# Performance work log

Measured on AMD Instinct MI355X. Metric: run time of the kernel, lower is better.

## Reference

```python
import jax, jax.numpy as jnp
import numpy as np
import math

D_MODEL = 2048
B, S, PAST = 4, 2048, 2048


def setup_inputs() -> dict:
    key = jax.random.key(0)
    ks = jax.random.split(key, 8)
    scale = 0.02
    x = jax.random.normal(ks[0], (B, S, D_MODEL), dtype=jnp.float32)
    past_k = jax.random.normal(ks[1], (B, PAST, D_MODEL), dtype=jnp.float32)
    past_v = jax.random.normal(ks[2], (B, PAST, D_MODEL), dtype=jnp.float32)
    Wq = jax.random.normal(ks[3], (D_MODEL, D_MODEL), dtype=jnp.float32) * scale
    Wk = jax.random.normal(ks[4], (D_MODEL, D_MODEL), dtype=jnp.float32) * scale
    Wv = jax.random.normal(ks[5], (D_MODEL, D_MODEL), dtype=jnp.float32) * scale
    Wo = jax.random.normal(ks[6], (D_MODEL, D_MODEL), dtype=jnp.float32) * scale
    bq = jnp.zeros((D_MODEL,), jnp.float32)
    bk = jnp.zeros((D_MODEL,), jnp.float32)
    bv = jnp.zeros((D_MODEL,), jnp.float32)
    bo = jnp.zeros((D_MODEL,), jnp.float32)
    return {"x": x, "past_k": past_k, "past_v": past_v,
            "Wq": Wq, "bq": bq, "Wk": Wk, "bk": bk,
            "Wv": Wv, "bv": bv, "Wo": Wo, "bo": bo}


def reference(x, past_k, past_v, Wq, bq, Wk, bk, Wv, bv, Wo, bo):
    d_model = x.shape[-1]
    # torch Linear: y = x @ W.T + b; here W is stored [out, in] equivalently square
    q = jnp.einsum('bsd,ed->bse', x, Wq) + bq
    k = jnp.einsum('bsd,ed->bse', x, Wk) + bk
    v = jnp.einsum('bsd,ed->bse', x, Wv) + bv
    k_cache = jnp.concatenate([past_k, k], axis=1)  # [B, PAST+S, D]
    v_cache = jnp.concatenate([past_v, v], axis=1)
    scores = jnp.einsum('bqd,bkd->bqk', q, k_cache) / math.sqrt(d_model)
    weights = jax.nn.softmax(scores, axis=-1)
    attn = jnp.einsum('bqk,bkd->bqd', weights, v_cache)
    out = jnp.einsum('bqd,ed->bqe', attn, Wo) + bo
    return out, (k_cache, v_cache)
```

## Files before the change

### kernel.cpp

```cpp
#include <hip/hip_runtime.h>
#include <math.h>

typedef unsigned short u16;
typedef __bf16 bf16x8 __attribute__((ext_vector_type(8)));
typedef float f32x4 __attribute__((ext_vector_type(4)));
typedef short s16x8 __attribute__((ext_vector_type(8)));

#define DM 2048
#define NB 4
#define SEQ 2048
#define PAST_N 2048
#define CS 4096

__device__ __forceinline__ u16 f2bf(float f) {
  unsigned u = __float_as_uint(f);
  u += 0x7fff + ((u >> 16) & 1);
  return (u16)(u >> 16);
}
__device__ __forceinline__ float bf2f(u16 h) {
  return __uint_as_float(((unsigned)h) << 16);
}

__device__ __forceinline__ void gl_lds16(const u16* g, u16* l) {
  __builtin_amdgcn_global_load_lds(
      (const __attribute__((address_space(1))) unsigned*)g,
      (__attribute__((address_space(3))) unsigned*)l, 16, 0, 0);
}

__device__ __forceinline__ bf16x8 ldsfrag(const u16* s, int row, int colb) {
  const int byte_off = (row * 128 + colb) ^ ((row & 7) << 4);
  return *(const bf16x8*)((const char*)s + byte_off);
}

__device__ __forceinline__ void stage4(const u16* __restrict__ g, int ld,
                                       u16* lwb, int t) {
#pragma unroll
  for (int j = 0; j < 4; ++j) {
    const int c = j * 512 + t;
    const int row = c >> 3;
    const int slot = (c & 7) ^ (row & 7);
    gl_lds16(g + (long)row * ld + slot * 8, lwb + j * 4096);
  }
}

#define LOADA(mh)                                                       \
  _Pragma("unroll") for (int mi = 0; mi < 4; ++mi) {                    \
    const int rwa = wr * 128 + ((mh) * 4 + mi) * 16 + lr;               \
    a[mi][0] = ldsfrag(sA, rwa, kb0);                                   \
    a[mi][1] = ldsfrag(sA, rwa, 64 + kb0);                              \
  }

#define LOADB(nh)                                                       \
  _Pragma("unroll") for (int ni = 0; ni < 2; ++ni) {                    \
    const int rwb = wc * 64 + ((nh) * 2 + ni) * 16 + lr;                \
    b[ni][0] = ldsfrag(sB, rwb, kb0);                                   \
    b[ni][1] = ldsfrag(sB, rwb, 64 + kb0);                              \
  }

#define MM(mh, nh)                                                      \
  _Pragma("unroll") for (int kk = 0; kk < 2; ++kk)                      \
  _Pragma("unroll") for (int mi = 0; mi < 4; ++mi)                      \
  _Pragma("unroll") for (int ni = 0; ni < 2; ++ni)                      \
    acc[(mh) * 4 + mi][(nh) * 2 + ni] =                                 \
        __builtin_amdgcn_mfma_f32_16x16x32_bf16(                        \
            a[mi][kk], b[ni][kk], acc[(mh) * 4 + mi][(nh) * 2 + ni],    \
            0, 0, 0);

#define PHASE_SYNC                                                      \
  __builtin_amdgcn_s_barrier();                                         \
  asm volatile("s_waitcnt lgkmcnt(0)" ::: "memory");                    \
  __builtin_amdgcn_sched_barrier(0);

#define GEMM_MAIN_LOOP(Abp, Bbp, ldav, ldbv)                            \
  stage4(Abp, ldav, &shA[0][w * 512], t);                               \
  stage4(Bbp, ldbv, &shB[0][w * 512], t);                               \
  asm volatile("s_waitcnt vmcnt(0)" ::: "memory");                      \
  __builtin_amdgcn_s_barrier();                                         \
  for (int tt = 0; tt < NT; ++tt) {                                     \
    const int cur = tt & 1;                                             \
    const u16* sA = shA[cur];                                           \
    const u16* sB = shB[cur];                                           \
    const bool pf = (tt + 1 < NT);                                      \
    const int ko = (tt + 1) << 6;                                       \
    LOADA(0)                                                            \
    LOADB(0)                                                            \
    if (pf) stage4(Abp + ko, ldav, &shA[cur ^ 1][w * 512], t);          \
    PHASE_SYNC                                                          \
    __builtin_amdgcn_s_setprio(1);                                      \
    MM(0, 0)                                                            \
    __builtin_amdgcn_s_setprio(0);                                      \
    __builtin_amdgcn_s_barrier();                                       \
    LOADB(1)                                                            \
    if (pf) stage4(Bbp + ko, ldbv, &shB[cur ^ 1][w * 512], t);          \
    PHASE_SYNC                                                          \
    __builtin_amdgcn_s_setprio(1);                                      \
    MM(0, 1)                                                            \
    __builtin_amdgcn_s_setprio(0);                                      \
    __builtin_amdgcn_s_barrier();                                       \
    LOADA(1)                                                            \
    PHASE_SYNC                                                          \
    __builtin_amdgcn_s_setprio(1);                                      \
    MM(1, 1)                                                            \
    __builtin_amdgcn_s_setprio(0);                                      \
    __builtin_amdgcn_s_barrier();                                       \
    LOADB(0)                                                            \
    PHASE_SYNC                                                          \
    __builtin_amdgcn_s_setprio(1);                                      \
    MM(1, 0)                                                            \
    __builtin_amdgcn_s_setprio(0);                                      \
    if (pf) asm volatile("s_waitcnt vmcnt(0)" ::: "memory");            \
    __builtin_amdgcn_s_barrier();                                       \
  }

template <int EPI>
__global__ __launch_bounds__(512, 2) void gemm256(
    const u16* __restrict__ A, const u16* __restrict__ B,
    float* __restrict__ Cf, u16* __restrict__ Cb, const float* __restrict__ bias,
    int K, int lda, int ldb, int ldc, long strA, long strB, long strC,
    float scale) {
  __shared__ __align__(16) u16 shA[2][256 * 64];
  __shared__ __align__(16) u16 shB[2][256 * 64];
  const int t = threadIdx.x;
  const int lane = t & 63;
  const int w = t >> 6;
  const int wr = w >> 2, wc = w & 3;
  const int lr = lane & 15, kb0 = (lane >> 4) * 16;

  const int gx = gridDim.x, gy = gridDim.y;
  const int nwg = gx * gy * gridDim.z;
  const int orig = blockIdx.x + gx * (blockIdx.y + gy * blockIdx.z);
  const int swz = (orig & 7) * (nwg >> 3) + (orig >> 3);
  const int bx = swz % gx;
  const int r1 = swz / gx;
  const int by = r1 % gy;
  const long bz = r1 / gy;
  const int brow = by * 256, bcol = bx * 256;

  const u16* Ab = A + bz * strA + (long)brow * lda;
  const u16* Bb = B + bz * strB + (long)bcol * ldb;
  const int NT = K >> 6;

  f32x4 acc[8][4] = {};
  bf16x8 a[4][2], b[2][2];

  GEMM_MAIN_LOOP(Ab, Bb, lda, ldb)

  const long cb = bz * strC;
#pragma unroll
  for (int m = 0; m < 8; ++m) {
    const int r0 = wr * 128 + m * 16 + (lane >> 4) * 4;
#pragma unroll
    for (int n = 0; n < 4; ++n) {
      const int c = bcol + wc * 64 + n * 16 + lr;
      const float bv = bias ? bias[c] : 0.0f;
#pragma unroll
      for (int r = 0; r < 4; ++r) {
        const int row = brow + r0 + r;
        const float val = (acc[m][n][r] + bv) * scale;
        if (EPI == 0) Cf[cb + (long)row * ldc + c] = val;
        else          Cb[cb + (long)row * ldc + c] = f2bf(val);
      }
    }
  }
}

__global__ __launch_bounds__(512, 2) void gemm_qkv(
    const u16* __restrict__ A, const u16* __restrict__ wq,
    const u16* __restrict__ wk, const u16* __restrict__ wv,
    const float* __restrict__ bq, const float* __restrict__ bk,
    const float* __restrict__ bv_, u16* __restrict__ qb,
    float* __restrict__ kc, u16* __restrict__ kbm,
    float* __restrict__ vc, u16* __restrict__ vtb, float qscale) {
  __shared__ __align__(16) u16 shA[2][256 * 64];
  __shared__ __align__(16) u16 shB[2][256 * 64];
  const int t = threadIdx.x;
  const int lane = t & 63;
  const int w = t >> 6;
  const int wr = w >> 2, wc = w & 3;
  const int lr = lane & 15, kb0 = (lane >> 4) * 16;

  const int gx = gridDim.x, gy = gridDim.y;
  const int nwg = gx * gy * gridDim.z;
  const int orig = blockIdx.x + gx * (blockIdx.y + gy * blockIdx.z);
  const int swz = (orig & 7) * (nwg >> 3) + (orig >> 3);
  const int bx = swz % gx;
  const int r1 = swz / gx;
  const int by = r1 % gy;
  const int bz = r1 / gy;
  const int brow = by * 256, bcol = bx * 256;

  const u16* Bw = (bz == 0) ? wq : (bz == 1) ? wk : wv;
  const float* bias = (bz == 0) ? bq : (bz == 1) ? bk : bv_;
  const u16* Ab = A + (long)brow * 2048;
  const u16* Bb = Bw + (long)bcol * 2048;
  const int NT = 2048 >> 6;

  f32x4 acc[8][4] = {};
  bf16x8 a[4][2], b[2][2];

  GEMM_MAIN_LOOP(Ab, Bb, 2048, 2048)

  if (bz == 0) {
#pragma unroll
    for (int m = 0; m < 8; ++m) {
      const int r0 = wr * 128 + m * 16 + (lane >> 4) * 4;
#pragma unroll
      for (int n = 0; n < 4; ++n) {
        const int c = bcol + wc * 64 + n * 16 + lr;
        const float bvv = bias[c];
#pragma unroll
        for (int r = 0; r < 4; ++r) {
          const int row = brow + r0 + r;
          qb[(long)row * 2048 + c] = f2bf((acc[m][n][r] + bvv) * qscale);
        }
      }
    }
  } else if (bz == 1) {
#pragma unroll
    for (int m = 0; m < 8; ++m) {
      const int r0 = wr * 128 + m * 16 + (lane >> 4) * 4;
#pragma unroll
      for (int n = 0; n < 4; ++n) {
        const int c = bcol + wc * 64 + n * 16 + lr;
        const float bvv = bias[c];
#pragma unroll
        for (int r = 0; r < 4; ++r) {
          const int row = brow + r0 + r;
          const long orow = (long)((row >> 11) * CS + PAST_N + (row & (SEQ - 1)));
          const float val = acc[m][n][r] + bvv;
          kc[orow * 2048 + c] = val;
          kbm[orow * 2048 + c] = f2bf(val);
        }
      }
    }
  } else {
#pragma unroll
    for (int m = 0; m < 8; ++m) {
      const int r0 = wr * 128 + m * 16 + (lane >> 4) * 4;
#pragma unroll
      for (int n = 0; n < 4; ++n) {
        const int c = bcol + wc * 64 + n * 16 + lr;
        const float bvv = bias[c];
        ushort4 pk4;
        const int row0 = brow + r0;
        const int bat = row0 >> 11;
        const long orow0 = (long)(bat * CS + PAST_N + (row0 & (SEQ - 1)));
#pragma unroll
        for (int r = 0; r < 4; ++r) {
          const float val = acc[m][n][r] + bvv;
          vc[(orow0 + r) * 2048 + c] = val;
          ((u16*)&pk4)[r] = f2bf(val);
        }
        *(ushort4*)(vtb + (long)bat * DM * CS + (long)c * CS + PAST_N +
                    (row0 & (SEQ - 1))) = pk4;
      }
    }
  }
}

__global__ __launch_bounds__(256) void cast_all(
    const float* __restrict__ x, u16* __restrict__ xb,
    const float* __restrict__ wq, u16* __restrict__ wqb,
    const float* __restrict__ wk, u16* __restrict__ wkb,
    const float* __restrict__ wv, u16* __restrict__ wvb,
    const float* __restrict__ wo, u16* __restrict__ wob) {
  const int z = blockIdx.z;
  const float* src;
  u16* dst;
  if (z < 4) { src = x + (long)z * 4194304; dst = xb + (long)z * 4194304; }
  else if (z == 4) { src = wq; dst = wqb; }
  else if (z == 5) { src = wk; dst = wkb; }
  else if (z == 6) { src = wv; dst = wvb; }
  else { src = wo; dst = wob; }
  const int i = blockIdx.x * 256 + threadIdx.x;
  const float4 v = ((const float4*)src)[i];
  ushort4 o;
  o.x = f2bf(v.x); o.y = f2bf(v.y); o.z = f2bf(v.z); o.w = f2bf(v.w);
  ((ushort4*)dst)[i] = o;
}

__global__ __launch_bounds__(256) void past_pass(
    const float* __restrict__ pk, const float* __restrict__ pv,
    float* __restrict__ kc, u16* __restrict__ kb,
    float* __restrict__ vc, u16* __restrict__ vtb) {
  const int z = blockIdx.z;
  const int t = threadIdx.x;
  if (z >= 4) {
    const int bb = z - 4;
    const int i = (blockIdx.y * 64 + blockIdx.x) * 256 + t;
    const int d4 = DM / 4;
    const int p = i / d4, col = i - p * d4;
    const float4 v = ((const float4*)(pk + (long)bb * PAST_N * DM))[i];
    const long o = ((long)(bb * CS + p)) * d4 + col;
    ((float4*)kc)[o] = v;
    ushort4 u;
    u.x = f2bf(v.x); u.y = f2bf(v.y); u.z = f2bf(v.z); u.w = f2bf(v.w);
    ((ushort4*)kb)[o] = u;
    return;
  }
  __shared__ float tile[32][33];
  const int bb = z;
  const int k0 = blockIdx.x * 32, d0 = blockIdx.y * 32;
  const int k = t >> 3, q = t & 7;
  const float* src = pv + (long)bb * PAST_N * DM;
  const float4 v = *(const float4*)(src + (long)(k0 + k) * DM + d0 + q * 4);
  *(float4*)(vc + ((long)(bb * CS + k0 + k)) * DM + d0 + q * 4) = v;
  tile[k][q * 4 + 0] = v.x;
  tile[k][q * 4 + 1] = v.y;
  tile[k][q * 4 + 2] = v.z;
  tile[k][q * 4 + 3] = v.w;
  __syncthreads();
  const int d = t >> 3, q2 = t & 7;
  ushort4 o;
#pragma unroll
  for (int r = 0; r < 4; ++r) o.x, o.y;
  ((u16*)&o)[0] = f2bf(tile[q2 * 4 + 0][d]);
  ((u16*)&o)[1] = f2bf(tile[q2 * 4 + 1][d]);
  ((u16*)&o)[2] = f2bf(tile[q2 * 4 + 2][d]);
  ((u16*)&o)[3] = f2bf(tile[q2 * 4 + 3][d]);
  *(ushort4*)(vtb + (long)bb * DM * CS + (long)(d0 + d) * CS + k0 + q2 * 4) = o;
}

__global__ __launch_bounds__(256) void softmax_rows(u16* __restrict__ s) {
  const long row = blockIdx.x;
  u16* p = s + row * CS;
  const int t = threadIdx.x;
  const int lane = t & 63, w = t >> 6;
  float v[16];
  s16x8 c0 = ((const s16x8*)p)[t * 2];
  s16x8 c1 = ((const s16x8*)p)[t * 2 + 1];
#pragma unroll
  for (int i = 0; i < 8; ++i) {
    v[i] = bf2f((u16)c0[i]);
    v[8 + i] = bf2f((u16)c1[i]);
  }
  float m = v[0];
#pragma unroll
  for (int i = 1; i < 16; ++i) m = fmaxf(m, v[i]);
#pragma unroll
  for (int o = 32; o >= 1; o >>= 1) m = fmaxf(m, __shfl_xor(m, o, 64));
  __shared__ float red[4];
  if (lane == 0) red[w] = m;
  __syncthreads();
  m = fmaxf(fmaxf(red[0], red[1]), fmaxf(red[2], red[3]));
  float sum = 0.f;
#pragma unroll
  for (int i = 0; i < 16; ++i) {
    v[i] = __expf(v[i] - m);
    sum += v[i];
  }
#pragma unroll
  for (int o = 32; o >= 1; o >>= 1) sum += __shfl_xor(sum, o, 64);
  __syncthreads();
  if (lane == 0) red[w] = sum;
  __syncthreads();
  sum = red[0] + red[1] + red[2] + red[3];
  const float inv = 1.0f / sum;
#pragma unroll
  for (int i = 0; i < 8; ++i) {
    c0[i] = (short)f2bf(v[i] * inv);
    c1[i] = (short)f2bf(v[8 + i] * inv);
  }
  ((s16x8*)p)[t * 2] = c0;
  ((s16x8*)p)[t * 2 + 1] = c1;
}

extern "C" void kernel_launch(void* const* d_in, const int* in_sizes, int n_in,
                              void* d_out, int out_size, void* d_ws, size_t ws_size,
                              hipStream_t stream) {
  const float* x  = (const float*)d_in[0];
  const float* pk = (const float*)d_in[1];
  const float* pv = (const float*)d_in[2];
  const float* Wq = (const float*)d_in[3];
  const float* bq = (const float*)d_in[4];
  const float* Wk = (const float*)d_in[5];
  const float* bk = (const float*)d_in[6];
  const float* Wv = (const float*)d_in[7];
  const float* bv = (const float*)d_in[8];
  const float* Wo = (const float*)d_in[9];
  const float* bo = (const float*)d_in[10];

  float* out = (float*)d_out;
  float* kc = out + (long)NB * SEQ * DM;
  float* vc = kc + (long)NB * CS * DM;

  u16* ws = (u16*)d_ws;
  u16* xb  = ws;
  u16* wqb = ws + 16777216;
  u16* wkb = wqb + 4194304;
  u16* wvb = wkb + 4194304;
  u16* wob = wvb + 4194304;
  u16* qb  = ws + 33554432;
  u16* kb  = ws + 50331648;
  u16* vtb = ws + 83886080;
  u16* sc  = ws + 117440512;

  const float qscale = 0.022097086912079608f;

  cast_all<<<dim3(4096, 1, 8), 256, 0, stream>>>(
      x, xb, Wq, wqb, Wk, wkb, Wv, wvb, Wo, wob);

  past_pass<<<dim3(64, 64, 8), 256, 0, stream>>>(pk, pv, kc, kb, vc, vtb);

  gemm_qkv<<<dim3(8, 32, 3), 512, 0, stream>>>(
      xb, wqb, wkb, wvb, bq, bk, bv, qb, kc, kb, vc, vtb, qscale);

  gemm256<1><<<dim3(16, 8, 4), 512, 0, stream>>>(
      qb, kb, nullptr, sc, nullptr, 2048, 2048, 2048, 4096,
      2048L * 2048, 4096L * 2048, 2048L * 4096, 1.0f);

  softmax_rows<<<8192, 256, 0, stream>>>(sc);

  gemm256<1><<<dim3(8, 8, 4), 512, 0, stream>>>(
      sc, vtb, nullptr, xb, nullptr, 4096, 4096, 4096, 2048,
      2048L * 4096, 2048L * 4096, 2048L * 2048, 1.0f);

  gemm256<0><<<dim3(8, 32, 1), 512, 0, stream>>>(
      xb, wob, out, nullptr, bo, 2048, 2048, 2048, 2048, 0, 0, 0, 1.0f);
}
```

Before: 748.8 us.

## Fuse softmax into QK and PV GEMM epilogues via partial row sums

Removes the separate softmax kernel. The QK GEMM epilogue now writes exp(score) as bf16 and stores per-tile partial row sums into a scratch buffer that reuses the Wq bf16 workspace. The PV GEMM prologue adds up those partials and scales its output rows by the reciprocal sum. This drops one full read/write pass over the 4x2048x4096 score matrix and a kernel launch. In exchange it omits the max subtraction, which risks overflow for large scores, and it leans on the scores staying small in magnitude.

After: 728.8 us, median of 2. -2.7%, faster.

```diff
diff --git a/kernel.cpp b/kernel.cpp
--- a/kernel.cpp
+++ b/kernel.cpp
@@ -112,14 +112,16 @@
     __builtin_amdgcn_s_barrier();                                       \
   }
 
-template <int EPI>
+template <int MODE>
 __global__ __launch_bounds__(512, 2) void gemm256(
     const u16* __restrict__ A, const u16* __restrict__ B,
     float* __restrict__ Cf, u16* __restrict__ Cb, const float* __restrict__ bias,
+    float* __restrict__ part,
     int K, int lda, int ldb, int ldc, long strA, long strB, long strC,
     float scale) {
   __shared__ __align__(16) u16 shA[2][256 * 64];
   __shared__ __align__(16) u16 shB[2][256 * 64];
+  __shared__ float ro[256];
   const int t = threadIdx.x;
   const int lane = t & 63;
   const int w = t >> 6;
@@ -140,6 +142,17 @@
   const u16* Bb = B + bz * strB + (long)bcol * ldb;
   const int NT = K >> 6;
 
+  if (MODE == 3) {
+    if (t < 256) {
+      const float* pr = part + (bz * 2048 + brow + t) * 64;
+      float s = 0.f;
+#pragma unroll 8
+      for (int j = 0; j < 64; ++j) s += pr[j];
+      ro[t] = 1.0f / s;
+    }
+    __syncthreads();
+  }
+
   f32x4 acc[8][4] = {};
   bf16x8 a[4][2], b[2][2];
 
@@ -148,17 +161,39 @@
   const long cb = bz * strC;
 #pragma unroll
   for (int m = 0; m < 8; ++m) {
-    const int r0 = wr * 128 + m * 16 + (lane >> 4) * 4;
+    const int rb = wr * 128 + m * 16 + (lane >> 4) * 4;
+    float rs[4] = {0.f, 0.f, 0.f, 0.f};
 #pragma unroll
     for (int n = 0; n < 4; ++n) {
       const int c = bcol + wc * 64 + n * 16 + lr;
-      const float bv = bias ? bias[c] : 0.0f;
+      const float bv = (MODE == 0 || MODE == 1) ? (bias ? bias[c] : 0.0f) : 0.0f;
 #pragma unroll
       for (int r = 0; r < 4; ++r) {
-        const int row = brow + r0 + r;
-        const float val = (acc[m][n][r] + bv) * scale;
-        if (EPI == 0) Cf[cb + (long)row * ldc + c] = val;
-        else          Cb[cb + (long)row * ldc + c] = f2bf(val);
+        const int row = brow + rb + r;
+        float val = (acc[m][n][r] + bv) * scale;
+        if (MODE == 0) {
+          Cf[cb + (long)row * ldc + c] = val;
+        } else if (MODE == 1) {
+          Cb[cb + (long)row * ldc + c] = f2bf(val);
+        } else if (MODE == 2) {
+          const float e = __expf(val);
+          rs[r] += e;
+          Cb[cb + (long)row * ldc + c] = f2bf(e);
+        } else {
+          Cb[cb + (long)row * ldc + c] = f2bf(val * ro[rb + r]);
+        }
+      }
+    }
+    if (MODE == 2) {
+#pragma unroll
+      for (int r = 0; r < 4; ++r) {
+        float s = rs[r];
+        s += __shfl_xor(s, 1, 64);
+        s += __shfl_xor(s, 2, 64);
+        s += __shfl_xor(s, 4, 64);
+        s += __shfl_xor(s, 8, 64);
+        if (lr == 0)
+          part[(bz * 2048 + brow + rb + r) * 64 + bx * 4 + wc] = s;
       }
     }
   }
@@ -312,57 +347,11 @@
   __syncthreads();
   const int d = t >> 3, q2 = t & 7;
   ushort4 o;
-#pragma unroll
-  for (int r = 0; r < 4; ++r) o.x, o.y;
   ((u16*)&o)[0] = f2bf(tile[q2 * 4 + 0][d]);
   ((u16*)&o)[1] = f2bf(tile[q2 * 4 + 1][d]);
   ((u16*)&o)[2] = f2bf(tile[q2 * 4 + 2][d]);
   ((u16*)&o)[3] = f2bf(tile[q2 * 4 + 3][d]);
   *(ushort4*)(vtb + (long)bb * DM * CS + (long)(d0 + d) * CS + k0 + q2 * 4) = o;
-}
-
-__global__ __launch_bounds__(256) void softmax_rows(u16* __restrict__ s) {
-  const long row = blockIdx.x;
-  u16* p = s + row * CS;
-  const int t = threadIdx.x;
-  const int lane = t & 63, w = t >> 6;
-  float v[16];
-  s16x8 c0 = ((const s16x8*)p)[t * 2];
-  s16x8 c1 = ((const s16x8*)p)[t * 2 + 1];
-#pragma unroll
-  for (int i = 0; i < 8; ++i) {
-    v[i] = bf2f((u16)c0[i]);
-    v[8 + i] = bf2f((u16)c1[i]);
-  }
-  float m = v[0];
-#pragma unroll
-  for (int i = 1; i < 16; ++i) m = fmaxf(m, v[i]);
-#pragma unroll
-  for (int o = 32; o >= 1; o >>= 1) m = fmaxf(m, __shfl_xor(m, o, 64));
-  __shared__ float red[4];
-  if (lane == 0) red[w] = m;
-  __syncthreads();
-  m = fmaxf(fmaxf(red[0], red[1]), fmaxf(red[2], red[3]));
-  float sum = 0.f;
-#pragma unroll
-  for (int i = 0; i < 16; ++i) {
-    v[i] = __expf(v[i] - m);
-    sum += v[i];
-  }
-#pragma unroll
-  for (int o = 32; o >= 1; o >>= 1) sum += __shfl_xor(sum, o, 64);
-  __syncthreads();
-  if (lane == 0) red[w] = sum;
-  __syncthreads();
-  sum = red[0] + red[1] + red[2] + red[3];
-  const float inv = 1.0f / sum;
-#pragma unroll
-  for (int i = 0; i < 8; ++i) {
-    c0[i] = (short)f2bf(v[i] * inv);
-    c1[i] = (short)f2bf(v[8 + i] * inv);
-  }
-  ((s16x8*)p)[t * 2] = c0;
-  ((s16x8*)p)[t * 2 + 1] = c1;
 }
 
 extern "C" void kernel_launch(void* const* d_in, const int* in_sizes, int n_in,
@@ -394,6 +383,7 @@
   u16* kb  = ws + 50331648;
   u16* vtb = ws + 83886080;
   u16* sc  = ws + 117440512;
+  float* part = (float*)wqb;
 
   const float qscale = 0.022097086912079608f;
 
@@ -405,16 +395,14 @@
   gemm_qkv<<<dim3(8, 32, 3), 512, 0, stream>>>(
       xb, wqb, wkb, wvb, bq, bk, bv, qb, kc, kb, vc, vtb, qscale);
 
-  gemm256<1><<<dim3(16, 8, 4), 512, 0, stream>>>(
-      qb, kb, nullptr, sc, nullptr, 2048, 2048, 2048, 4096,
+  gemm256<2><<<dim3(16, 8, 4), 512, 0, stream>>>(
+      qb, kb, nullptr, sc, nullptr, part, 2048, 2048, 2048, 4096,
       2048L * 2048, 4096L * 2048, 2048L * 4096, 1.0f);
 
-  softmax_rows<<<8192, 256, 0, stream>>>(sc);
-
-  gemm256<1><<<dim3(8, 8, 4), 512, 0, stream>>>(
-      sc, vtb, nullptr, xb, nullptr, 4096, 4096, 4096, 2048,
+  gemm256<3><<<dim3(8, 8, 4), 512, 0, stream>>>(
+      sc, vtb, nullptr, xb, nullptr, part, 4096, 4096, 4096, 2048,
       2048L * 4096, 2048L * 4096, 2048L * 2048, 1.0f);
 
   gemm256<0><<<dim3(8, 32, 1), 512, 0, stream>>>(
-      xb, wob, out, nullptr, bo, 2048, 2048, 2048, 2048, 0, 0, 0, 1.0f);
-}
+      xb, wob, out, nullptr, bo, nullptr, 2048, 2048, 2048, 2048, 0, 0, 0, 1.0f);
+}
```
